# Kernel optimization log

Hardware: AMD Instinct MI355X
Metric: run time of the kernel (lower is better)

Reference implementation:

```python
import jax, jax.numpy as jnp
import numpy as np

NPOINT = 2048
NSAMPLE = 16
IN_CH = 64
OUT_CH = 128
LEAKY = 0.1
EPS = 1e-5


def leaky(x):
    return jnp.where(x >= 0, x, LEAKY * x)


def bn_train(x, g, b):
    # training-mode BatchNorm2d over (B, S, K) per channel; x: [B,C,S,K]
    m = jnp.mean(x, axis=(0, 2, 3), keepdims=True)
    v = jnp.var(x, axis=(0, 2, 3), keepdims=True)
    return (x - m) * jax.lax.rsqrt(v + EPS) * g.reshape(1, -1, 1, 1) + b.reshape(1, -1, 1, 1)


def fps(xyz, npoint):
    # furthest point sampling, xyz: [B,N,3], starts at index 0 (matches pointnet2)
    B, N, _ = xyz.shape
    def step(carry, _):
        dist, last = carry
        pt = jnp.take_along_axis(xyz, last[:, None, None], axis=1)  # [B,1,3]
        d = jnp.sum((xyz - pt) ** 2, axis=-1)                       # [B,N]
        dist = jnp.minimum(dist, d)
        nxt = jnp.argmax(dist, axis=-1).astype(jnp.int32)
        return (dist, nxt), nxt
    init = (jnp.full((B, N), 1e10, xyz.dtype), jnp.zeros((B,), jnp.int32))
    _, idxs = jax.lax.scan(step, init, None, length=npoint - 1)
    return jnp.concatenate([jnp.zeros((1, B), jnp.int32), idxs], axis=0).T  # [B,npoint]


def knn(nsample, xyz, new_xyz):
    # xyz: [B,N,3], new_xyz: [B,S,3] -> [B,S,nsample]
    sqr = (jnp.sum(new_xyz ** 2, -1)[:, :, None]
           + jnp.sum(xyz ** 2, -1)[:, None, :]
           - 2.0 * jnp.einsum('bsc,bnc->bsn', new_xyz, xyz))
    _, idx = jax.lax.top_k(-sqr, nsample)
    return idx


def gather_pts(points, idx):
    # points: [B,N,C], idx: [B,...] -> [B,...,C]
    return jax.vmap(lambda p, i: p[i])(points, idx)


def setup_inputs() -> dict:
    key = jax.random.key(0)
    ks = jax.random.split(key, 16)
    B, N = 4, 8192
    h = OUT_CH // 2
    sc = lambda fan: 1.0 / np.sqrt(fan)
    return {
        'xyz': jax.random.normal(ks[0], (B, 3, N), jnp.float32),
        'points': jax.random.normal(ks[1], (B, IN_CH, N), jnp.float32),
        'W0': jax.random.normal(ks[2], (IN_CH, h), jnp.float32) * sc(IN_CH),
        'b0': jnp.zeros((h,), jnp.float32),
        'g0': jnp.ones((h,), jnp.float32),
        'be0': jnp.zeros((h,), jnp.float32),
        'W1': jax.random.normal(ks[3], (9, h), jnp.float32) * sc(9),
        'b1': jnp.zeros((h,), jnp.float32),
        'g1': jnp.ones((h,), jnp.float32),
        'be1': jnp.zeros((h,), jnp.float32),
        'Ws': jax.random.normal(ks[4], (OUT_CH, OUT_CH), jnp.float32) * sc(OUT_CH),
        'W2': jax.random.normal(ks[5], (OUT_CH, OUT_CH), jnp.float32) * sc(OUT_CH),
        'b2': jnp.zeros((OUT_CH,), jnp.float32),
        'g2': jnp.ones((OUT_CH,), jnp.float32),
        'be2': jnp.zeros((OUT_CH,), jnp.float32),
    }


def reference(xyz, points, W0, b0, g0, be0, W1, b1, g1, be1, Ws, W2, b2, g2, be2):
    B = xyz.shape[0]
    xyz_t = jnp.transpose(xyz, (0, 2, 1))      # [B,N,3]
    pts_t = jnp.transpose(points, (0, 2, 1))   # [B,N,D]

    fps_idx = fps(xyz_t, NPOINT)               # [B,S]
    new_xyz = gather_pts(xyz_t, fps_idx)       # [B,S,3]
    idx = knn(NSAMPLE, xyz_t, new_xyz)         # [B,S,K]

    grouped_xyz = gather_pts(xyz_t, idx)                      # [B,S,K,3]
    grouped_xyz_norm = grouped_xyz - new_xyz[:, :, None, :]   # [B,S,K,3]
    grouped_points = gather_pts(pts_t, idx)                   # [B,S,K,D]

    # mlp0: 1x1 conv + BN + leaky  -> [B,h,S,K]
    new_points = leaky(bn_train(
        jnp.einsum('bskd,dc->bcsk', grouped_points, W0) + b0.reshape(1, -1, 1, 1), g0, be0))

    extended = jnp.broadcast_to(jnp.transpose(new_xyz, (0, 2, 1))[..., None],
                                (B, 3, NPOINT, NSAMPLE))
    concat = jnp.concatenate([extended,
                              jnp.transpose(grouped_xyz, (0, 3, 1, 2)),
                              jnp.transpose(grouped_xyz_norm, (0, 3, 1, 2))], axis=1)  # [B,9,S,K]

    lse_part = leaky(bn_train(
        jnp.einsum('bcsk,cd->bdsk', concat, W1) + b1.reshape(1, -1, 1, 1), g1, be1))
    lse1 = jnp.concatenate([lse_part, new_points], axis=1)    # [B,out,S,K]

    # score_fn1: 1x1 conv (no bias) -> leaky -> softmax over nsample
    scores = jax.nn.softmax(leaky(jnp.einsum('bcsk,cd->bdsk', lse1, Ws)), axis=-1)
    features1 = jnp.sum(scores * lse1, axis=-1, keepdims=True)  # [B,out,S,1]

    new_points_out = leaky(bn_train(
        jnp.einsum('bcsk,cd->bdsk', features1, W2) + b2.reshape(1, -1, 1, 1), g2, be2))
    new_points_out = jnp.squeeze(new_points_out, -1)            # [B,out,S]

    return jnp.transpose(new_xyz, (0, 2, 1)), new_points_out, fps_idx
```

## Files before the change

### kernel.cpp

```cpp
#include <hip/hip_runtime.h>

#define BB 4
#define NN 8192
#define SS 2048
#define KK 16
#define INCH 64
#define HH 64
#define OUTC 128
#define LEAKY_A 0.1f
#define EPSF 1e-5f

__device__ __forceinline__ float sq3(float a, float b, float c) {
    return __fadd_rn(__fadd_rn(__fmul_rn(a, a), __fmul_rn(b, b)), __fmul_rn(c, c));
}

__device__ __forceinline__ float leaky_f(float x) { return x >= 0.f ? x : LEAKY_A * x; }

__device__ __forceinline__ int spread3(int v) {
    return (v & 1) | ((v & 2) << 2) | ((v & 4) << 4);
}

__device__ __forceinline__ unsigned long long shfl_xor_u64(unsigned long long v, int off) {
    unsigned lo = (unsigned)v, hi = (unsigned)(v >> 32);
    lo = __shfl_xor(lo, off);
    hi = __shfl_xor(hi, off);
    return ((unsigned long long)hi << 32) | lo;
}

__global__ __launch_bounds__(1024)
void fps_kernel(const float* __restrict__ xyz,
                int* __restrict__ fps_idx,
                float* __restrict__ new_xyz,
                float* __restrict__ out0,
                float* __restrict__ out2)
{
    int b = blockIdx.x, t = threadIdx.x;
    int lane = t & 63, wid = t >> 6;
    const float* xb = xyz + (long)b * 3 * NN;

    __shared__ unsigned short perm[NN];
    __shared__ unsigned int hist[512];
    __shared__ unsigned int starts[512];
    __shared__ unsigned int wsum[8];
    __shared__ float wred[16][6];
    __shared__ unsigned long long skey[2][16];
    __shared__ float4 sval[2][16];
    __shared__ unsigned short pick[SS];

    float lx[8], ly[8], lz[8];
    float mnx = 3.4e38f, mny = 3.4e38f, mnz = 3.4e38f;
    float mxx = -3.4e38f, mxy = -3.4e38f, mxz = -3.4e38f;
#pragma unroll
    for (int j = 0; j < 8; ++j) {
        int n = t * 8 + j;
        lx[j] = xb[n]; ly[j] = xb[NN + n]; lz[j] = xb[2 * NN + n];
        mnx = fminf(mnx, lx[j]); mxx = fmaxf(mxx, lx[j]);
        mny = fminf(mny, ly[j]); mxy = fmaxf(mxy, ly[j]);
        mnz = fminf(mnz, lz[j]); mxz = fmaxf(mxz, lz[j]);
    }
#pragma unroll
    for (int off = 1; off < 64; off <<= 1) {
        mnx = fminf(mnx, __shfl_xor(mnx, off)); mxx = fmaxf(mxx, __shfl_xor(mxx, off));
        mny = fminf(mny, __shfl_xor(mny, off)); mxy = fmaxf(mxy, __shfl_xor(mxy, off));
        mnz = fminf(mnz, __shfl_xor(mnz, off)); mxz = fmaxf(mxz, __shfl_xor(mxz, off));
    }
    if (lane == 0) {
        wred[wid][0] = mnx; wred[wid][1] = mny; wred[wid][2] = mnz;
        wred[wid][3] = mxx; wred[wid][4] = mxy; wred[wid][5] = mxz;
    }
    if (t < 512) hist[t] = 0;
    __syncthreads();
    mnx = wred[0][0]; mny = wred[0][1]; mnz = wred[0][2];
    mxx = wred[0][3]; mxy = wred[0][4]; mxz = wred[0][5];
#pragma unroll
    for (int w = 1; w < 16; ++w) {
        mnx = fminf(mnx, wred[w][0]); mny = fminf(mny, wred[w][1]); mnz = fminf(mnz, wred[w][2]);
        mxx = fmaxf(mxx, wred[w][3]); mxy = fmaxf(mxy, wred[w][4]); mxz = fmaxf(mxz, wred[w][5]);
    }
    float sclx = 8.0f / fmaxf(mxx - mnx, 1e-9f);
    float scly = 8.0f / fmaxf(mxy - mny, 1e-9f);
    float sclz = 8.0f / fmaxf(mxz - mnz, 1e-9f);
    int mcode[8];
#pragma unroll
    for (int j = 0; j < 8; ++j) {
        int ux = (int)((lx[j] - mnx) * sclx); ux = ux < 0 ? 0 : (ux > 7 ? 7 : ux);
        int uy = (int)((ly[j] - mny) * scly); uy = uy < 0 ? 0 : (uy > 7 ? 7 : uy);
        int uz = (int)((lz[j] - mnz) * sclz); uz = uz < 0 ? 0 : (uz > 7 ? 7 : uz);
        mcode[j] = spread3(ux) | (spread3(uy) << 1) | (spread3(uz) << 2);
        atomicAdd(&hist[mcode[j]], 1u);
    }
    __syncthreads();
    unsigned v = 0, incl = 0;
    if (t < 512) {
        v = hist[t];
        incl = v;
#pragma unroll
        for (int d = 1; d < 64; d <<= 1) {
            unsigned u = __shfl_up(incl, d);
            if (lane >= d) incl += u;
        }
        if (lane == 63) wsum[wid] = incl;
    }
    __syncthreads();
    if (t < 512) {
        unsigned off = 0;
        for (int w = 0; w < wid; ++w) off += wsum[w];
        starts[t] = off + incl - v;
    }
    __syncthreads();
#pragma unroll
    for (int j = 0; j < 8; ++j) {
        unsigned pos = atomicAdd(&starts[mcode[j]], 1u);
        perm[pos] = (unsigned short)(t * 8 + j);
    }
    __syncthreads();

    float px[8], py[8], pz[8], dist[8];
    int oi[8];
#pragma unroll
    for (int j = 0; j < 8; ++j) {
        int o = perm[t * 8 + j];
        oi[j] = o;
        px[j] = xb[o]; py[j] = xb[NN + o]; pz[j] = xb[2 * NN + o];
        dist[j] = 1e10f;
    }
#define CSWAP(a, b) { if (oi[a] > oi[b]) { int ti = oi[a]; oi[a] = oi[b]; oi[b] = ti; \
    float tf; tf = px[a]; px[a] = px[b]; px[b] = tf; \
    tf = py[a]; py[a] = py[b]; py[b] = tf; \
    tf = pz[a]; pz[a] = pz[b]; pz[b] = tf; } }
    CSWAP(0,1) CSWAP(2,3) CSWAP(4,5) CSWAP(6,7)
    CSWAP(0,2) CSWAP(1,3) CSWAP(4,6) CSWAP(5,7)
    CSWAP(1,2) CSWAP(5,6)
    CSWAP(0,4) CSWAP(1,5) CSWAP(2,6) CSWAP(3,7)
    CSWAP(2,4) CSWAP(3,5)
    CSWAP(1,2) CSWAP(3,4) CSWAP(5,6)
#undef CSWAP
    float tbx0 = 3.4e38f, tby0 = 3.4e38f, tbz0 = 3.4e38f;
    float tbx1 = -3.4e38f, tby1 = -3.4e38f, tbz1 = -3.4e38f;
#pragma unroll
    for (int j = 0; j < 8; ++j) {
        tbx0 = fminf(tbx0, px[j]); tbx1 = fmaxf(tbx1, px[j]);
        tby0 = fminf(tby0, py[j]); tby1 = fmaxf(tby1, py[j]);
        tbz0 = fminf(tbz0, pz[j]); tbz1 = fmaxf(tbz1, pz[j]);
    }

    unsigned kh = __float_as_uint(1e10f), kl = 0u;
    float bx = 0.f, by = 0.f, bz = 0.f;
    bool iswin = false;

    if (t == 0) pick[0] = 0;
    float cx = xb[0], cy = xb[NN], cz = xb[2 * NN];

#define DPPMAX(m, CTRL) { \
    unsigned _o = (unsigned)__builtin_amdgcn_update_dpp(0, (int)(m), CTRL, 0xf, 0xf, true); \
    (m) = (_o > (m)) ? _o : (m); \
}

    for (int i = 1; i < SS; ++i) {
        float gx = fmaxf(fmaxf(tbx0 - cx, cx - tbx1), 0.f);
        float gy = fmaxf(fmaxf(tby0 - cy, cy - tby1), 0.f);
        float gz = fmaxf(fmaxf(tbz0 - cz, cz - tbz1), 0.f);
        float lb = gx * gx + gy * gy + gz * gz;
        bool thr_act = lb <= __uint_as_float(kh) * 1.00001f;
        if (__any((int)thr_act)) {
            if (thr_act) {
                float bv = -1.f; int bi = 0; float nbx = 0.f, nby = 0.f, nbz = 0.f;
#pragma unroll
                for (int j = 0; j < 8; ++j) {
                    float dx = __fsub_rn(px[j], cx), dy = __fsub_rn(py[j], cy), dz = __fsub_rn(pz[j], cz);
                    float d = sq3(dx, dy, dz);
                    float nd = fminf(dist[j], d);
                    dist[j] = nd;
                    if (nd > bv) { bv = nd; bi = oi[j]; nbx = px[j]; nby = py[j]; nbz = pz[j]; }
                }
                kh = __float_as_uint(bv); kl = ~(unsigned)bi;
                bx = nbx; by = nby; bz = nbz;
            }
            unsigned m = kh;
            DPPMAX(m, 0x111) DPPMAX(m, 0x112) DPPMAX(m, 0x114)
            DPPMAX(m, 0x118) DPPMAX(m, 0x142) DPPMAX(m, 0x143)
            unsigned wmax = (unsigned)__builtin_amdgcn_readlane((int)m, 63);
            unsigned long long mask = __ballot((int)(kh == wmax));
            int wlane;
            if (__popcll(mask) == 1) {
                wlane = (int)__builtin_ctzll(mask);
            } else {
                unsigned t2 = (kh == wmax) ? kl : 0u;
                DPPMAX(t2, 0x111) DPPMAX(t2, 0x112) DPPMAX(t2, 0x114)
                DPPMAX(t2, 0x118) DPPMAX(t2, 0x142) DPPMAX(t2, 0x143)
                unsigned klm = (unsigned)__builtin_amdgcn_readlane((int)t2, 63);
                wlane = (int)__builtin_ctzll(__ballot((int)(kh == wmax && kl == klm)));
            }
            iswin = (lane == wlane);
        }
        int buf = i & 1;
        if (iswin) {
            skey[buf][wid] = ((unsigned long long)kh << 32) | kl;
            sval[buf][wid] = make_float4(bx, by, bz, 0.f);
        }
        __syncthreads();
        unsigned long long sk = skey[buf][lane & 15];
        float4 sv = sval[buf][lane & 15];
        unsigned xh = (unsigned)(sk >> 32), xl = (unsigned)sk;
        unsigned m2 = xh;
        DPPMAX(m2, 0x111) DPPMAX(m2, 0x112) DPPMAX(m2, 0x114) DPPMAX(m2, 0x118)
        unsigned wh = (unsigned)__builtin_amdgcn_readlane((int)m2, 15);
        unsigned long long mk = __ballot((int)(lane < 16 && xh == wh));
        int widx;
        if (__popcll(mk) == 1) {
            widx = (int)__builtin_ctzll(mk);
        } else {
            unsigned t3 = (lane < 16 && xh == wh) ? xl : 0u;
            DPPMAX(t3, 0x111) DPPMAX(t3, 0x112) DPPMAX(t3, 0x114) DPPMAX(t3, 0x118)
            unsigned wl2 = (unsigned)__builtin_amdgcn_readlane((int)t3, 15);
            widx = (int)__builtin_ctzll(__ballot((int)(lane < 16 && xh == wh && xl == wl2)));
        }
        cx = __shfl(sv.x, widx);
        cy = __shfl(sv.y, widx);
        cz = __shfl(sv.z, widx);
        unsigned wl = (unsigned)__shfl((int)xl, widx);
        if (t == 0) pick[i] = (unsigned short)(~wl);
    }
#undef DPPMAX
    __syncthreads();
    for (int i = t; i < SS; i += 1024) {
        int n = pick[i];
        float x = xb[n], y = xb[NN + n], z = xb[2 * NN + n];
        new_xyz[((long)b * SS + i) * 3 + 0] = x;
        new_xyz[((long)b * SS + i) * 3 + 1] = y;
        new_xyz[((long)b * SS + i) * 3 + 2] = z;
        out0[(long)b * 3 * SS + 0 * SS + i] = x;
        out0[(long)b * 3 * SS + 1 * SS + i] = y;
        out0[(long)b * 3 * SS + 2 * SS + i] = z;
        out2[b * SS + i] = (float)n;
    }
}

__global__ __launch_bounds__(256)
void knn_kernel(const float* __restrict__ xyz,
                const float* __restrict__ new_xyz,
                int* __restrict__ knn_idx)
{
    int gwave = (blockIdx.x * 256 + threadIdx.x) >> 6;
    int lane = threadIdx.x & 63;
    if (gwave >= BB * SS) return;
    int b = gwave / SS;
    const float* xb = xyz + (long)b * 3 * NN;
    float nx = new_xyz[(long)gwave * 3 + 0];
    float ny = new_xyz[(long)gwave * 3 + 1];
    float nz = new_xyz[(long)gwave * 3 + 2];
    float snew = sq3(nx, ny, nz);
    unsigned long long kk[16];
    const unsigned long long KINIT = 0xFF7FFFFF7FFFFFFFull;
#pragma unroll
    for (int j = 0; j < 16; ++j) kk[j] = KINIT;
    unsigned long long wk = KINIT; int ws = 0;
    for (int tix = 0; tix < NN / 64; ++tix) {
        int n = tix * 64 + lane;
        float qx = xb[n], qy = xb[NN + n], qz = xb[2 * NN + n];
        float sx = sq3(qx, qy, qz);
        float dot = __fadd_rn(__fadd_rn(__fmul_rn(nx, qx), __fmul_rn(ny, qy)), __fmul_rn(nz, qz));
        float d = __fsub_rn(__fadd_rn(snew, sx), __fmul_rn(2.0f, dot));
        unsigned ud = __float_as_uint(d);
        ud = ((int)ud < 0) ? ~ud : (ud | 0x80000000u);
        unsigned long long key = ((unsigned long long)ud << 32) | (unsigned)n;
        if (key < wk) {
            kk[ws] = key;
            wk = kk[0]; ws = 0;
#pragma unroll
            for (int j = 1; j < 16; ++j) {
                bool g = kk[j] > wk;
                wk = g ? kk[j] : wk; ws = g ? j : ws;
            }
        }
    }
    int myres = 0;
#pragma unroll
    for (int r = 0; r < 16; ++r) {
        unsigned long long mn = kk[0]; int ms = 0;
#pragma unroll
        for (int j = 1; j < 16; ++j) {
            bool l = kk[j] < mn;
            mn = l ? kk[j] : mn; ms = l ? j : ms;
        }
        unsigned long long bm = mn;
#pragma unroll
        for (int off = 1; off < 64; off <<= 1) {
            unsigned long long om = shfl_xor_u64(bm, off);
            if (om < bm) bm = om;
        }
        if (mn == bm) kk[ms] = 0xFFFFFFFFFFFFFFFFull;
        if (lane == r) myres = (int)(unsigned)(bm & 0xffffffffull);
    }
    if (lane < 16) knn_idx[(long)gwave * 16 + lane] = myres;
}

__global__ __launch_bounds__(256)
void mlp01_stats_kernel(const float* __restrict__ points,
                        const float* __restrict__ xyz,
                        const float* __restrict__ new_xyz,
                        const int* __restrict__ knn_idx,
                        const float* __restrict__ W0, const float* __restrict__ b0,
                        const float* __restrict__ W1, const float* __restrict__ b1,
                        float* __restrict__ sums)
{
    int wid = threadIdx.x >> 6, lane = threadIdx.x & 63;
    int xcd = blockIdx.x & 7;
    int b = xcd >> 1;
    int idx_in_b = ((blockIdx.x >> 3) << 1) + (xcd & 1);
    long base = ((long)b * 512 + idx_in_b) * 64 + wid * 16;
    const float* pb = points + (long)b * INCH * NN + (long)lane * NN;
    const float* xb = xyz + (long)b * 3 * NN;
    float a0 = 0, q0 = 0, a1 = 0, q1 = 0;
#pragma unroll
    for (int half = 0; half < 2; ++half) {
        int ns[8]; float gps[8];
#pragma unroll
        for (int j = 0; j < 8; ++j) ns[j] = knn_idx[base + half * 8 + j];
#pragma unroll
        for (int j = 0; j < 8; ++j) gps[j] = pb[ns[j]];
#pragma unroll
        for (int j = 0; j < 8; ++j) {
            long pos = base + half * 8 + j;
            int bs = (int)(pos >> 4);
            int n = ns[j];
            float gp = gps[j];
            float x0 = b0[lane];
#pragma unroll
            for (int d = 0; d < 64; ++d)
                x0 = fmaf(__shfl(gp, d), W0[d * 64 + lane], x0);
            float nx = new_xyz[(long)bs * 3], ny = new_xyz[(long)bs * 3 + 1], nz = new_xyz[(long)bs * 3 + 2];
            float qx = xb[n], qy = xb[NN + n], qz = xb[2 * NN + n];
            float c9[9] = {nx, ny, nz, qx, qy, qz, qx - nx, qy - ny, qz - nz};
            float x1 = b1[lane];
#pragma unroll
            for (int jj = 0; jj < 9; ++jj) x1 = fmaf(c9[jj], W1[jj * 64 + lane], x1);
            a0 += x0; q0 += x0 * x0; a1 += x1; q1 += x1 * x1;
        }
    }
    __shared__ float red[4][4][64];
    red[0][wid][lane] = a0; red[1][wid][lane] = q0; red[2][wid][lane] = a1; red[3][wid][lane] = q1;
    __syncthreads();
    if (threadIdx.x < 64) {
#pragma unroll
        for (int arr = 0; arr < 4; ++arr) {
            float v = red[arr][0][lane] + red[arr][1][lane] + red[arr][2][lane] + red[arr][3][lane];
            atomicAdd(&sums[arr * 64 + lane], v);
        }
    }
}

__global__ void bn01_finalize(const float* __restrict__ sums,
                              const float* __restrict__ g0, const float* __restrict__ be0,
                              const float* __restrict__ g1, const float* __restrict__ be1,
                              float* __restrict__ ss01)
{
    int c = threadIdx.x;
    float inv = 1.0f / (float)(BB * SS * KK);
    float m0 = sums[c] * inv,        v0 = sums[64 + c] * inv - m0 * m0;
    float m1 = sums[128 + c] * inv,  v1 = sums[192 + c] * inv - m1 * m1;
    float sc0 = g0[c] / sqrtf(v0 + EPSF);
    float sc1 = g1[c] / sqrtf(v1 + EPSF);
    ss01[c] = sc0;        ss01[64 + c] = be0[c] - m0 * sc0;
    ss01[128 + c] = sc1;  ss01[192 + c] = be1[c] - m1 * sc1;
}

__global__ __launch_bounds__(256)
void center_kernel(const float* __restrict__ points, const float* __restrict__ xyz,
                   const float* __restrict__ new_xyz, const int* __restrict__ knn_idx,
                   const float* __restrict__ W0, const float* __restrict__ b0,
                   const float* __restrict__ W1, const float* __restrict__ b1,
                   const float* __restrict__ ss01, const float* __restrict__ Ws,
                   float* __restrict__ features1)
{
    int xcd = blockIdx.x & 7;
    int b = xcd >> 1;
    int s = ((blockIdx.x >> 3) << 1) + (xcd & 1);
    int bs = (b << 11) + s;
    int wid = threadIdx.x >> 6, lane = threadIdx.x & 63;
    __shared__ float lse[KK][OUTC];
    __shared__ float sraw[KK][OUTC];
    float sc0 = ss01[lane], sh0 = ss01[64 + lane], sc1 = ss01[128 + lane], sh1 = ss01[192 + lane];
    float nx = new_xyz[(long)bs * 3], ny = new_xyz[(long)bs * 3 + 1], nz = new_xyz[(long)bs * 3 + 2];
    const float* xb = xyz + (long)b * 3 * NN;
    const float* pb = points + (long)b * INCH * NN + (long)lane * NN;
    int n4[4]; float gp4[4];
#pragma unroll
    for (int kk = 0; kk < 4; ++kk) n4[kk] = knn_idx[(long)bs * 16 + wid * 4 + kk];
#pragma unroll
    for (int kk = 0; kk < 4; ++kk) gp4[kk] = pb[n4[kk]];
#pragma unroll
    for (int kk = 0; kk < 4; ++kk) {
        int k = wid * 4 + kk;
        int n = n4[kk];
        float gp = gp4[kk];
        float x0 = b0[lane];
#pragma unroll
        for (int d = 0; d < 64; ++d)
            x0 = fmaf(__shfl(gp, d), W0[d * 64 + lane], x0);
        float qx = xb[n], qy = xb[NN + n], qz = xb[2 * NN + n];
        float c9[9] = {nx, ny, nz, qx, qy, qz, qx - nx, qy - ny, qz - nz};
        float x1 = b1[lane];
#pragma unroll
        for (int j = 0; j < 9; ++j) x1 = fmaf(c9[j], W1[j * 64 + lane], x1);
        x0 = leaky_f(x0 * sc0 + sh0);
        x1 = leaky_f(x1 * sc1 + sh1);
        lse[k][lane] = x1;
        lse[k][64 + lane] = x0;
    }
    __syncthreads();
    int d = threadIdx.x & 127;
    int kg = threadIdx.x >> 7;
    float acc[8];
#pragma unroll
    for (int i = 0; i < 8; ++i) acc[i] = 0.f;
    for (int c = 0; c < OUTC; ++c) {
        float w = Ws[c * OUTC + d];
#pragma unroll
        for (int i = 0; i < 8; ++i) acc[i] = fmaf(lse[kg * 8 + i][c], w, acc[i]);
    }
#pragma unroll
    for (int i = 0; i < 8; ++i) sraw[kg * 8 + i][d] = leaky_f(acc[i]);
    __syncthreads();
    if (threadIdx.x < OUTC) {
        int dd = threadIdx.x;
        float vals[KK];
        float mx = -3.4e38f;
#pragma unroll
        for (int k = 0; k < KK; ++k) { vals[k] = sraw[k][dd]; mx = fmaxf(mx, vals[k]); }
        float sum = 0.f;
#pragma unroll
        for (int k = 0; k < KK; ++k) { vals[k] = __expf(vals[k] - mx); sum += vals[k]; }
        float invs = 1.0f / sum;
        float feat = 0.f;
#pragma unroll
        for (int k = 0; k < KK; ++k) feat = fmaf(vals[k] * invs, lse[k][dd], feat);
        features1[(long)bs * OUTC + dd] = feat;
    }
}

__global__ __launch_bounds__(256)
void mlp2_kernel(const float* __restrict__ features1,
                 const float* __restrict__ W2, const float* __restrict__ b2,
                 float* __restrict__ x2,
                 float* __restrict__ sums2)
{
    int p0 = blockIdx.x * 16;
    __shared__ float f[16][OUTC];
    for (int i = threadIdx.x; i < 16 * OUTC; i += 256)
        f[i >> 7][i & 127] = features1[(long)p0 * OUTC + i];
    __syncthreads();
    int d = threadIdx.x & 127;
    int g = threadIdx.x >> 7;
    float acc[8];
#pragma unroll
    for (int i = 0; i < 8; ++i) acc[i] = b2[d];
    for (int c = 0; c < OUTC; ++c) {
        float w = W2[c * OUTC + d];
#pragma unroll
        for (int i = 0; i < 8; ++i) acc[i] = fmaf(f[g * 8 + i][c], w, acc[i]);
    }
    float s = 0.f, q = 0.f;
#pragma unroll
    for (int i = 0; i < 8; ++i) {
        x2[(long)(p0 + g * 8 + i) * OUTC + d] = acc[i];
        s += acc[i]; q += acc[i] * acc[i];
    }
    __shared__ float rs[2][2][OUTC];
    rs[0][g][d] = s; rs[1][g][d] = q;
    __syncthreads();
    if (threadIdx.x < OUTC) {
        atomicAdd(&sums2[d],        rs[0][0][d] + rs[0][1][d]);
        atomicAdd(&sums2[OUTC + d], rs[1][0][d] + rs[1][1][d]);
    }
}

__global__ void bn2_finalize(const float* __restrict__ sums2,
                             const float* __restrict__ g2, const float* __restrict__ be2,
                             float* __restrict__ ss2)
{
    int c = threadIdx.x;
    float inv = 1.0f / (float)(BB * SS);
    float m = sums2[c] * inv, v = sums2[OUTC + c] * inv - m * m;
    float sc = g2[c] / sqrtf(v + EPSF);
    ss2[c] = sc; ss2[OUTC + c] = be2[c] - m * sc;
}

__global__ __launch_bounds__(256)
void out1_kernel(const float* __restrict__ x2, const float* __restrict__ ss2,
                 float* __restrict__ out1)
{
    int bc = blockIdx.x;
    int b = bc >> 7, c = bc & 127;
    float sc = ss2[c], sh = ss2[OUTC + c];
    for (int s = threadIdx.x; s < SS; s += 256) {
        float v = x2[((long)(b * SS + s)) * OUTC + c] * sc + sh;
        out1[(long)b * OUTC * SS + (long)c * SS + s] = leaky_f(v);
    }
}

extern "C" void kernel_launch(void* const* d_in, const int* in_sizes, int n_in,
                              void* d_out, int out_size, void* d_ws, size_t ws_size,
                              hipStream_t stream)
{
    const float* xyz    = (const float*)d_in[0];
    const float* points = (const float*)d_in[1];
    const float* W0  = (const float*)d_in[2];
    const float* b0  = (const float*)d_in[3];
    const float* g0  = (const float*)d_in[4];
    const float* be0 = (const float*)d_in[5];
    const float* W1  = (const float*)d_in[6];
    const float* b1  = (const float*)d_in[7];
    const float* g1  = (const float*)d_in[8];
    const float* be1 = (const float*)d_in[9];
    const float* Ws  = (const float*)d_in[10];
    const float* W2  = (const float*)d_in[11];
    const float* b2  = (const float*)d_in[12];
    const float* g2  = (const float*)d_in[13];
    const float* be2 = (const float*)d_in[14];

    char* ws = (char*)d_ws;
    int*   fps_i  = (int*)(ws + 0);
    float* nxyz   = (float*)(ws + 32768);
    int*   knn_i  = (int*)(ws + 131072);
    float* sums01 = (float*)(ws + 655360);
    float* sums2  = (float*)(ws + 656384);
    float* ss01   = (float*)(ws + 657408);
    float* ss2    = (float*)(ws + 658432);
    float* feat1  = (float*)(ws + 659456);
    float* x2     = (float*)(ws + 659456 + 4194304);

    float* out0 = (float*)d_out;
    float* out1 = out0 + (long)BB * 3 * SS;
    float* out2 = out1 + (long)BB * OUTC * SS;

    hipMemsetAsync(sums01, 0, 2048, stream);

    fps_kernel<<<BB, 1024, 0, stream>>>(xyz, fps_i, nxyz, out0, out2);
    knn_kernel<<<(BB * SS) / 4, 256, 0, stream>>>(xyz, nxyz, knn_i);
    mlp01_stats_kernel<<<2048, 256, 0, stream>>>(points, xyz, nxyz, knn_i, W0, b0, W1, b1, sums01);
    bn01_finalize<<<1, 64, 0, stream>>>(sums01, g0, be0, g1, be1, ss01);
    center_kernel<<<BB * SS, 256, 0, stream>>>(points, xyz, nxyz, knn_i, W0, b0, W1, b1, ss01, Ws, feat1);
    mlp2_kernel<<<(BB * SS) / 16, 256, 0, stream>>>(feat1, W2, b2, x2, sums2);
    bn2_finalize<<<1, 128, 0, stream>>>(sums2, g2, be2, ss2);
    out1_kernel<<<BB * OUTC, 256, 0, stream>>>(x2, ss2, out1);
}
```

Before: 2.427 ms.

## Fuse BN0/1 stats into knn kernel and inline BN finalize into consumers

The first-layer batchnorm statistics computation moves into the knn kernel, with each wave using its freshly computed neighbor indices via shuffles instead of re-reading them in a separate kernel. The two small BN finalize kernels are removed: each consumer block recomputes scale and shift from the raw sums. This cuts three kernel launches and a global round trip of knn indices. In exchange the knn waves do extra work and every consumer block redundantly recomputes the finalize.

```diff
diff --git a/kernel.cpp b/kernel.cpp
--- a/kernel.cpp
+++ b/kernel.cpp
@@ -29,7 +29,6 @@
 
 __global__ __launch_bounds__(1024)
 void fps_kernel(const float* __restrict__ xyz,
-                int* __restrict__ fps_idx,
                 float* __restrict__ new_xyz,
                 float* __restrict__ out0,
                 float* __restrict__ out2)
@@ -239,11 +238,15 @@
 __global__ __launch_bounds__(256)
 void knn_kernel(const float* __restrict__ xyz,
                 const float* __restrict__ new_xyz,
-                int* __restrict__ knn_idx)
+                int* __restrict__ knn_idx,
+                const float* __restrict__ points,
+                const float* __restrict__ W0, const float* __restrict__ b0,
+                const float* __restrict__ W1, const float* __restrict__ b1,
+                float* __restrict__ sums)
 {
     int gwave = (blockIdx.x * 256 + threadIdx.x) >> 6;
     int lane = threadIdx.x & 63;
-    if (gwave >= BB * SS) return;
+    int wid = threadIdx.x >> 6;
     int b = gwave / SS;
     const float* xb = xyz + (long)b * 3 * NN;
     float nx = new_xyz[(long)gwave * 3 + 0];
@@ -293,50 +296,23 @@
         if (lane == r) myres = (int)(unsigned)(bm & 0xffffffffull);
     }
     if (lane < 16) knn_idx[(long)gwave * 16 + lane] = myres;
-}
-
-__global__ __launch_bounds__(256)
-void mlp01_stats_kernel(const float* __restrict__ points,
-                        const float* __restrict__ xyz,
-                        const float* __restrict__ new_xyz,
-                        const int* __restrict__ knn_idx,
-                        const float* __restrict__ W0, const float* __restrict__ b0,
-                        const float* __restrict__ W1, const float* __restrict__ b1,
-                        float* __restrict__ sums)
-{
-    int wid = threadIdx.x >> 6, lane = threadIdx.x & 63;
-    int xcd = blockIdx.x & 7;
-    int b = xcd >> 1;
-    int idx_in_b = ((blockIdx.x >> 3) << 1) + (xcd & 1);
-    long base = ((long)b * 512 + idx_in_b) * 64 + wid * 16;
+
     const float* pb = points + (long)b * INCH * NN + (long)lane * NN;
-    const float* xb = xyz + (long)b * 3 * NN;
     float a0 = 0, q0 = 0, a1 = 0, q1 = 0;
 #pragma unroll
-    for (int half = 0; half < 2; ++half) {
-        int ns[8]; float gps[8];
-#pragma unroll
-        for (int j = 0; j < 8; ++j) ns[j] = knn_idx[base + half * 8 + j];
-#pragma unroll
-        for (int j = 0; j < 8; ++j) gps[j] = pb[ns[j]];
-#pragma unroll
-        for (int j = 0; j < 8; ++j) {
-            long pos = base + half * 8 + j;
-            int bs = (int)(pos >> 4);
-            int n = ns[j];
-            float gp = gps[j];
-            float x0 = b0[lane];
-#pragma unroll
-            for (int d = 0; d < 64; ++d)
-                x0 = fmaf(__shfl(gp, d), W0[d * 64 + lane], x0);
-            float nx = new_xyz[(long)bs * 3], ny = new_xyz[(long)bs * 3 + 1], nz = new_xyz[(long)bs * 3 + 2];
-            float qx = xb[n], qy = xb[NN + n], qz = xb[2 * NN + n];
-            float c9[9] = {nx, ny, nz, qx, qy, qz, qx - nx, qy - ny, qz - nz};
-            float x1 = b1[lane];
-#pragma unroll
-            for (int jj = 0; jj < 9; ++jj) x1 = fmaf(c9[jj], W1[jj * 64 + lane], x1);
-            a0 += x0; q0 += x0 * x0; a1 += x1; q1 += x1 * x1;
-        }
+    for (int k = 0; k < 16; ++k) {
+        int n = __shfl(myres, k);
+        float gp = pb[n];
+        float x0 = b0[lane];
+#pragma unroll
+        for (int d = 0; d < 64; ++d)
+            x0 = fmaf(__shfl(gp, d), W0[d * 64 + lane], x0);
+        float qx = xb[n], qy = xb[NN + n], qz = xb[2 * NN + n];
+        float c9[9] = {nx, ny, nz, qx, qy, qz, qx - nx, qy - ny, qz - nz};
+        float x1 = b1[lane];
+#pragma unroll
+        for (int j = 0; j < 9; ++j) x1 = fmaf(c9[j], W1[j * 64 + lane], x1);
+        a0 += x0; q0 += x0 * x0; a1 += x1; q1 += x1 * x1;
     }
     __shared__ float red[4][4][64];
     red[0][wid][lane] = a0; red[1][wid][lane] = q0; red[2][wid][lane] = a1; red[3][wid][lane] = q1;
@@ -348,21 +324,6 @@
             atomicAdd(&sums[arr * 64 + lane], v);
         }
     }
-}
-
-__global__ void bn01_finalize(const float* __restrict__ sums,
-                              const float* __restrict__ g0, const float* __restrict__ be0,
-                              const float* __restrict__ g1, const float* __restrict__ be1,
-                              float* __restrict__ ss01)
-{
-    int c = threadIdx.x;
-    float inv = 1.0f / (float)(BB * SS * KK);
-    float m0 = sums[c] * inv,        v0 = sums[64 + c] * inv - m0 * m0;
-    float m1 = sums[128 + c] * inv,  v1 = sums[192 + c] * inv - m1 * m1;
-    float sc0 = g0[c] / sqrtf(v0 + EPSF);
-    float sc1 = g1[c] / sqrtf(v1 + EPSF);
-    ss01[c] = sc0;        ss01[64 + c] = be0[c] - m0 * sc0;
-    ss01[128 + c] = sc1;  ss01[192 + c] = be1[c] - m1 * sc1;
 }
 
 __global__ __launch_bounds__(256)
@@ -370,7 +331,10 @@
                    const float* __restrict__ new_xyz, const int* __restrict__ knn_idx,
                    const float* __restrict__ W0, const float* __restrict__ b0,
                    const float* __restrict__ W1, const float* __restrict__ b1,
-                   const float* __restrict__ ss01, const float* __restrict__ Ws,
+                   const float* __restrict__ sums01,
+                   const float* __restrict__ g0, const float* __restrict__ be0,
+                   const float* __restrict__ g1, const float* __restrict__ be1,
+                   const float* __restrict__ Ws,
                    float* __restrict__ features1)
 {
     int xcd = blockIdx.x & 7;
@@ -380,7 +344,19 @@
     int wid = threadIdx.x >> 6, lane = threadIdx.x & 63;
     __shared__ float lse[KK][OUTC];
     __shared__ float sraw[KK][OUTC];
-    float sc0 = ss01[lane], sh0 = ss01[64 + lane], sc1 = ss01[128 + lane], sh1 = ss01[192 + lane];
+    __shared__ float ssl[4][64];
+    if (threadIdx.x < 64) {
+        int c = threadIdx.x;
+        float inv = 1.0f / (float)(BB * SS * KK);
+        float m0 = sums01[c] * inv,        v0 = sums01[64 + c] * inv - m0 * m0;
+        float m1 = sums01[128 + c] * inv,  v1 = sums01[192 + c] * inv - m1 * m1;
+        float s0 = g0[c] / sqrtf(v0 + EPSF);
+        float s1 = g1[c] / sqrtf(v1 + EPSF);
+        ssl[0][c] = s0; ssl[1][c] = be0[c] - m0 * s0;
+        ssl[2][c] = s1; ssl[3][c] = be1[c] - m1 * s1;
+    }
+    __syncthreads();
+    float sc0 = ssl[0][lane], sh0 = ssl[1][lane], sc1 = ssl[2][lane], sh1 = ssl[3][lane];
     float nx = new_xyz[(long)bs * 3], ny = new_xyz[(long)bs * 3 + 1], nz = new_xyz[(long)bs * 3 + 2];
     const float* xb = xyz + (long)b * 3 * NN;
     const float* pb = points + (long)b * INCH * NN + (long)lane * NN;
@@ -475,27 +451,20 @@
     }
 }
 
-__global__ void bn2_finalize(const float* __restrict__ sums2,
-                             const float* __restrict__ g2, const float* __restrict__ be2,
-                             float* __restrict__ ss2)
-{
-    int c = threadIdx.x;
-    float inv = 1.0f / (float)(BB * SS);
-    float m = sums2[c] * inv, v = sums2[OUTC + c] * inv - m * m;
-    float sc = g2[c] / sqrtf(v + EPSF);
-    ss2[c] = sc; ss2[OUTC + c] = be2[c] - m * sc;
-}
-
 __global__ __launch_bounds__(256)
-void out1_kernel(const float* __restrict__ x2, const float* __restrict__ ss2,
+void out1_kernel(const float* __restrict__ x2, const float* __restrict__ sums2,
+                 const float* __restrict__ g2, const float* __restrict__ be2,
                  float* __restrict__ out1)
 {
     int bc = blockIdx.x;
     int b = bc >> 7, c = bc & 127;
-    float sc = ss2[c], sh = ss2[OUTC + c];
+    float inv = 1.0f / (float)(BB * SS);
+    float m = sums2[c] * inv, v = sums2[OUTC + c] * inv - m * m;
+    float sc = g2[c] / sqrtf(v + EPSF);
+    float sh = be2[c] - m * sc;
     for (int s = threadIdx.x; s < SS; s += 256) {
-        float v = x2[((long)(b * SS + s)) * OUTC + c] * sc + sh;
-        out1[(long)b * OUTC * SS + (long)c * SS + s] = leaky_f(v);
+        float val = x2[((long)(b * SS + s)) * OUTC + c] * sc + sh;
+        out1[(long)b * OUTC * SS + (long)c * SS + s] = leaky_f(val);
     }
 }
 
@@ -520,13 +489,10 @@
     const float* be2 = (const float*)d_in[14];
 
     char* ws = (char*)d_ws;
-    int*   fps_i  = (int*)(ws + 0);
     float* nxyz   = (float*)(ws + 32768);
     int*   knn_i  = (int*)(ws + 131072);
     float* sums01 = (float*)(ws + 655360);
     float* sums2  = (float*)(ws + 656384);
-    float* ss01   = (float*)(ws + 657408);
-    float* ss2    = (float*)(ws + 658432);
     float* feat1  = (float*)(ws + 659456);
     float* x2     = (float*)(ws + 659456 + 4194304);
 
@@ -536,12 +502,10 @@
 
     hipMemsetAsync(sums01, 0, 2048, stream);
 
-    fps_kernel<<<BB, 1024, 0, stream>>>(xyz, fps_i, nxyz, out0, out2);
-    knn_kernel<<<(BB * SS) / 4, 256, 0, stream>>>(xyz, nxyz, knn_i);
-    mlp01_stats_kernel<<<2048, 256, 0, stream>>>(points, xyz, nxyz, knn_i, W0, b0, W1, b1, sums01);
-    bn01_finalize<<<1, 64, 0, stream>>>(sums01, g0, be0, g1, be1, ss01);
-    center_kernel<<<BB * SS, 256, 0, stream>>>(points, xyz, nxyz, knn_i, W0, b0, W1, b1, ss01, Ws, feat1);
+    fps_kernel<<<BB, 1024, 0, stream>>>(xyz, nxyz, out0, out2);
+    knn_kernel<<<(BB * SS) / 4, 256, 0, stream>>>(xyz, nxyz, knn_i, points, W0, b0, W1, b1, sums01);
+    center_kernel<<<BB * SS, 256, 0, stream>>>(points, xyz, nxyz, knn_i, W0, b0, W1, b1,
+                                               sums01, g0, be0, g1, be1, Ws, feat1);
     mlp2_kernel<<<(BB * SS) / 16, 256, 0, stream>>>(feat1, W2, b2, x2, sums2);
-    bn2_finalize<<<1, 128, 0, stream>>>(sums2, g2, be2, ss2);
-    out1_kernel<<<BB * OUTC, 256, 0, stream>>>(x2, ss2, out1);
-}
+    out1_kernel<<<BB * OUTC, 256, 0, stream>>>(x2, sums2, g2, be2, out1);
+}
```

After: 2.418 ms. About the same (-0.3%).
